# Kernel optimization log

Hardware: AMD Instinct MI355X
Metric: run time of the kernel (lower is better)

The kernel has to match this reference:

```python
import jax, jax.numpy as jnp
import numpy as np

N, E, D, G = 20000, 640000, 256, 64
BN_EPS = 1e-5


def setup_inputs() -> dict:
    key = jax.random.key(0)
    ks = jax.random.split(key, 16)
    p = lambda k, sh: jax.random.normal(k, sh, dtype=jnp.float32) * 0.05
    x = jax.random.normal(ks[0], (N, D), dtype=jnp.float32)
    edge_index = jax.random.randint(ks[1], (2, E), 0, N, dtype=jnp.int32)
    batch = jnp.sort(jax.random.randint(ks[2], (N,), 0, G, dtype=jnp.int32))
    return dict(
        x=x, edge_index=edge_index, batch=batch,
        W1=p(ks[3], (D, D)), a1_src=p(ks[4], (D,)), a1_dst=p(ks[5], (D,)), b1=p(ks[6], (D,)),
        W2=p(ks[7], (D, D)), a2_src=p(ks[8], (D,)), a2_dst=p(ks[9], (D,)), b2=p(ks[10], (D,)),
        bn_gamma=jnp.ones((D,), jnp.float32), bn_beta=jnp.zeros((D,), jnp.float32),
        bn_mean=jnp.zeros((D,), jnp.float32), bn_var=jnp.ones((D,), jnp.float32),
        Wl=p(ks[11], (D, D)), bl=p(ks[12], (D,)),
    )


def gat_conv(x, src, dst, W, a_src, a_dst, b):
    # PyG GATConv, heads=1, concat=True, negative_slope=0.2, self-loops already appended
    h = x @ W                               # [N, D]
    alpha_s = h @ a_src                     # [N]
    alpha_d = h @ a_dst                     # [N]
    e = jax.nn.leaky_relu(alpha_s[src] + alpha_d[dst], 0.2)   # [E+N]
    # segment softmax over edges grouped by destination node
    m = jax.ops.segment_max(e, dst, num_segments=N)
    ex = jnp.exp(e - m[dst])
    s = jax.ops.segment_sum(ex, dst, num_segments=N)
    alpha = ex / s[dst]                     # self-loops guarantee s > 0
    out = jax.ops.segment_sum(alpha[:, None] * h[src], dst, num_segments=N)
    return out + b


def reference(x, edge_index, batch, W1, a1_src, a1_dst, b1, W2, a2_src, a2_dst, b2,
              bn_gamma, bn_beta, bn_mean, bn_var, Wl, bl):
    loop = jnp.arange(N, dtype=edge_index.dtype)
    src = jnp.concatenate([edge_index[0], loop])
    dst = jnp.concatenate([edge_index[1], loop])

    h = jax.nn.leaky_relu(gat_conv(x, src, dst, W1, a1_src, a1_dst, b1), 0.01)
    h = jax.nn.leaky_relu(gat_conv(h, src, dst, W2, a2_src, a2_dst, b2), 0.01)
    # BatchNorm over nodes (eval mode, running stats)
    h = (h - bn_mean) * jax.lax.rsqrt(bn_var + BN_EPS) * bn_gamma + bn_beta
    # global mean pool per graph, then linear (dropout is identity in eval)
    sums = jax.ops.segment_sum(h, batch, num_segments=G)           # [G, D]
    cnt = jax.ops.segment_sum(jnp.ones((N,), h.dtype), batch, num_segments=G)
    pooled = sums / jnp.maximum(cnt, 1.0)[:, None]
    return pooled @ Wl.T + bl
```

## Files before the change

### kernel.cpp

```cpp
#include <hip/hip_runtime.h>
#include <hip/hip_bf16.h>

#define NN 20000
#define EE 640000
#define DD 256
#define GG 64
#define ETOT (EE + NN)
#define BN_EPS 1e-5f

#define NPART 8
#define PBLK  128
#define CE    (EE / PBLK)
#define PRNG  (NN / NPART)

#define GBM 64
#define GBN 128
#define GBK 64
#define NGEMMB 626
#define SCHUNKS 78
#define SCSZ 8206

typedef short s16x8 __attribute__((ext_vector_type(8)));
typedef float f32x4 __attribute__((ext_vector_type(4)));
typedef int   i32x2 __attribute__((ext_vector_type(2)));
typedef int   i32x4 __attribute__((ext_vector_type(4)));

__device__ __forceinline__ unsigned short f2bf_hi(float x) {
    unsigned u = __float_as_uint(x);
    unsigned r = (u + 0x7FFFu + ((u >> 16) & 1u)) >> 16;
    return (unsigned short)r;
}
__device__ __forceinline__ float bf2f(unsigned short h) {
    return __uint_as_float(((unsigned)h) << 16);
}

__device__ __forceinline__ void fma8o(const char* __restrict__ hbF, int boff,
                                      float a, float* acc) {
    i32x4 hv = *(const i32x4*)(hbF + boff);
    #pragma unroll
    for (int k = 0; k < 4; ++k) {
        unsigned u = (unsigned)hv[k];
        acc[2 * k]     += a * __uint_as_float(u << 16);
        acc[2 * k + 1] += a * __uint_as_float(u & 0xFFFF0000u);
    }
}

__global__ __launch_bounds__(256) void prep_hist_conv_kernel(
        const int* __restrict__ batch, int* __restrict__ start, float* __restrict__ cntf,
        const int* __restrict__ ei, int* __restrict__ counts,
        const float* __restrict__ W1, const float* __restrict__ W2,
        short* __restrict__ BhT1, short* __restrict__ BlT1,
        short* __restrict__ BhT2, short* __restrict__ BlT2) {
    int b = blockIdx.x;
    int r = b & 15, G = b >> 4;
    if (r < 8) {
        int lo = (b & 7) * PRNG;
        int e0 = G * CE;
        for (int i = e0 + threadIdx.x; i < e0 + CE; i += 256) {
            int d = ei[EE + i];
            if ((unsigned)(d - lo) < (unsigned)PRNG) atomicAdd(&counts[d], 1);
        }
        return;
    }
    int idx = G * 8 + (r - 8);
    if (idx < 512) {
        int n = idx & 255, which = idx >> 8;
        int k = threadIdx.x;
        const float* B = which ? W2 : W1;
        short* Bh = which ? BhT2 : BhT1;
        short* Bl = which ? BlT2 : BlT1;
        float x = B[k * DD + n];
        unsigned short hbv = f2bf_hi(x);
        Bh[n * DD + k] = (short)hbv;
        Bl[n * DD + k] = (short)f2bf_hi(x - bf2f(hbv));
    } else if (idx == 512) {
        int g = threadIdx.x;
        if (g <= GG) {
            if (g == GG) start[GG] = NN;
            else {
                int lo = 0, hi = NN;
                while (lo < hi) { int mid = (lo + hi) >> 1; if (batch[mid] < g) lo = mid + 1; else hi = mid; }
                start[g] = lo;
            }
        }
        __syncthreads();
        if (g < GG) cntf[g] = (float)(start[g + 1] - start[g]);
    }
}

#define SCHUNK 20
__global__ __launch_bounds__(1024) void scan_kernel(const int* __restrict__ counts,
                                                    int* __restrict__ offsets,
                                                    int* __restrict__ cursor) {
    __shared__ int wsums[16];
    int t = threadIdx.x, lane = t & 63, wid = t >> 6;
    int base = t * SCHUNK;
    int loc[SCHUNK];
    int sum = 0;
    #pragma unroll
    for (int i = 0; i < SCHUNK; ++i) {
        int idx = base + i;
        int v = (idx < NN) ? (counts[idx] + 1) : 0;
        loc[i] = sum; sum += v;
    }
    int x = sum;
    #pragma unroll
    for (int o = 1; o < 64; o <<= 1) { int tv = __shfl_up(x, o, 64); if (lane >= o) x += tv; }
    if (lane == 63) wsums[wid] = x;
    __syncthreads();
    if (wid == 0) {
        int wv = (lane < 16) ? wsums[lane] : 0;
        #pragma unroll
        for (int o = 1; o < 16; o <<= 1) { int tv = __shfl_up(wv, o, 64); if (lane >= o) wv += tv; }
        if (lane < 16) wsums[lane] = wv;
    }
    __syncthreads();
    int tbase = (wid ? wsums[wid - 1] : 0) + x - sum;
    #pragma unroll
    for (int i = 0; i < SCHUNK; ++i) {
        int idx = base + i;
        if (idx < NN) { int e = tbase + loc[i]; offsets[idx] = e; cursor[idx] = e; }
    }
    if (t == 0) offsets[NN] = wsums[15];
}

template<bool SCAT>
__global__ __launch_bounds__(256) void gemm_kernel(
        const float* __restrict__ A,
        const short* __restrict__ BhT, const short* __restrict__ BlT,
        const float* __restrict__ a_src, const float* __restrict__ a_dst,
        short* __restrict__ hb, float* __restrict__ asp, float* __restrict__ adp, int M,
        const int* __restrict__ ei, int* __restrict__ cursor, int* __restrict__ csr_src) {
    __shared__ short As_h[GBM * GBK];
    __shared__ short As_l[GBM * GBK];
    __shared__ short Bs_h[GBN * GBK];
    __shared__ short Bs_l[GBN * GBK];
    int tid = threadIdx.x;
    int lid = blockIdx.x;
    int gx = lid & 1, gy = lid >> 1;
    int row0 = gy * GBM;
    int col0 = gx * GBN;
    int w = tid >> 6, lane = tid & 63;
    int wr = w >> 1, wc = w & 1;

    f32x4 acc[2][4];
    #pragma unroll
    for (int m = 0; m < 2; ++m)
        #pragma unroll
        for (int n = 0; n < 4; ++n)
            acc[m][n] = (f32x4){0.f, 0.f, 0.f, 0.f};

    int srow = tid >> 3;
    int sslot = tid & 7;

    for (int k0 = 0; k0 < DD; k0 += GBK) {
        __syncthreads();
        #pragma unroll
        for (int p = 0; p < 2; ++p) {
            int r = p * 32 + srow;
            int gr = row0 + r;
            float xv[8];
            if (gr < M) {
                const float4* ap = (const float4*)(A + (size_t)gr * DD + k0 + sslot * 8);
                float4 a0 = ap[0], a1 = ap[1];
                xv[0] = a0.x; xv[1] = a0.y; xv[2] = a0.z; xv[3] = a0.w;
                xv[4] = a1.x; xv[5] = a1.y; xv[6] = a1.z; xv[7] = a1.w;
            } else {
                #pragma unroll
                for (int i = 0; i < 8; ++i) xv[i] = 0.f;
            }
            s16x8 hv, lv;
            #pragma unroll
            for (int i = 0; i < 8; ++i) {
                unsigned short hbb = f2bf_hi(xv[i]);
                hv[i] = (short)hbb;
                lv[i] = (short)f2bf_hi(xv[i] - bf2f(hbb));
            }
            int byte = r * 128 + ((sslot ^ (r & 7)) << 4);
            *(s16x8*)((char*)As_h + byte) = hv;
            *(s16x8*)((char*)As_l + byte) = lv;
        }
        #pragma unroll
        for (int p = 0; p < 4; ++p) {
            int r = p * 32 + srow;
            int byte = r * 128 + ((sslot ^ (r & 7)) << 4);
            const short* bhp = BhT + (size_t)(col0 + r) * DD + k0 + sslot * 8;
            const short* blp = BlT + (size_t)(col0 + r) * DD + k0 + sslot * 8;
            *(s16x8*)((char*)Bs_h + byte) = *(const s16x8*)bhp;
            *(s16x8*)((char*)Bs_l + byte) = *(const s16x8*)blp;
        }
        __syncthreads();

        #pragma unroll
        for (int ks = 0; ks < 2; ++ks) {
            s16x8 ah[2], al[2], bh[4], bl[4];
            int g = ks * 4 + (lane >> 4);
            #pragma unroll
            for (int m = 0; m < 2; ++m) {
                int r = wr * 32 + m * 16 + (lane & 15);
                int byte = r * 128 + ((g ^ (r & 7)) << 4);
                ah[m] = *(const s16x8*)((char*)As_h + byte);
                al[m] = *(const s16x8*)((char*)As_l + byte);
            }
            #pragma unroll
            for (int n = 0; n < 4; ++n) {
                int c = wc * 64 + n * 16 + (lane & 15);
                int byte = c * 128 + ((g ^ (c & 7)) << 4);
                bh[n] = *(const s16x8*)((char*)Bs_h + byte);
                bl[n] = *(const s16x8*)((char*)Bs_l + byte);
            }
            #pragma unroll
            for (int m = 0; m < 2; ++m)
                #pragma unroll
                for (int n = 0; n < 4; ++n) {
                    acc[m][n] = __builtin_amdgcn_mfma_f32_16x16x32_bf16(ah[m], bh[n], acc[m][n], 0, 0, 0);
                    acc[m][n] = __builtin_amdgcn_mfma_f32_16x16x32_bf16(ah[m], bl[n], acc[m][n], 0, 0, 0);
                    acc[m][n] = __builtin_amdgcn_mfma_f32_16x16x32_bf16(al[m], bh[n], acc[m][n], 0, 0, 0);
                }
        }
    }

    float vsrc[4], vdst[4];
    #pragma unroll
    for (int n = 0; n < 4; ++n) {
        int cg = col0 + wc * 64 + n * 16 + (lane & 15);
        vsrc[n] = a_src[cg];
        vdst[n] = a_dst[cg];
    }
    #pragma unroll
    for (int m = 0; m < 2; ++m) {
        #pragma unroll
        for (int j = 0; j < 4; ++j) {
            float ps = 0.f, pd = 0.f;
            #pragma unroll
            for (int n = 0; n < 4; ++n) {
                float c = acc[m][n][j];
                ps += c * vsrc[n];
                pd += c * vdst[n];
            }
            #pragma unroll
            for (int o = 1; o < 16; o <<= 1) {
                ps += __shfl_xor(ps, o, 64);
                pd += __shfl_xor(pd, o, 64);
            }
            if ((lane & 15) == 0) {
                int rg = row0 + wr * 32 + m * 16 + ((lane >> 4) << 2) + j;
                if (rg < M) {
                    asp[(size_t)(gx * 2 + wc) * NN + rg] = ps;
                    adp[(size_t)(gx * 2 + wc) * NN + rg] = pd;
                }
            }
        }
    }

    #pragma unroll
    for (int m = 0; m < 2; ++m) {
        int rbase = row0 + wr * 32 + m * 16 + ((lane >> 4) << 2);
        #pragma unroll
        for (int n = 0; n < 4; ++n) {
            int cg = col0 + wc * 64 + n * 16 + (lane & 15);
            #pragma unroll
            for (int j = 0; j < 4; ++j) {
                int rg = rbase + j;
                if (rg < M) hb[(size_t)rg * DD + cg] = (short)f2bf_hi(acc[m][n][j]);
            }
        }
    }

    if (SCAT && lid < SCHUNKS * NPART) {
        int part = lid & 7;
        int lo = part * PRNG;
        int e0 = (lid >> 3) * SCSZ;
        int e1 = min(e0 + SCSZ, EE);
        for (int i = e0 + tid; i < e1; i += 256) {
            int d = ei[EE + i];
            if ((unsigned)(d - lo) < (unsigned)PRNG) {
                int pos = atomicAdd(&cursor[d], 1);
                csr_src[pos] = ei[i];
            }
        }
    }
}

__global__ void reduce_kernel(const float* __restrict__ asp, const float* __restrict__ adp,
                              const int* __restrict__ offsets,
                              float* __restrict__ as_, float* __restrict__ ad_,
                              int* __restrict__ csr_src) {
    int i = blockIdx.x * blockDim.x + threadIdx.x;
    if (i < NN) {
        as_[i] = asp[i] + asp[NN + i] + asp[2 * NN + i] + asp[3 * NN + i];
        ad_[i] = adp[i] + adp[NN + i] + adp[2 * NN + i] + adp[3 * NN + i];
        csr_src[offsets[i + 1] - 1] = i;
    }
}

__global__ __launch_bounds__(256) void alpha_kernel(const int* __restrict__ csr_src,
                                                    const int* __restrict__ offsets,
                                                    const float* __restrict__ as_,
                                                    const float* __restrict__ ad_,
                                                    int2* __restrict__ pairs) {
    int tid = threadIdx.x;
    int w = tid >> 6, lane = tid & 63;
    int node = blockIdx.x * 4 + w;
    int off = offsets[node];
    int deg = offsets[node + 1] - off;
    float adn = ad_[node];

    if (deg <= 64) {
        int si = 0; float e = -INFINITY;
        if (lane < deg) {
            si = csr_src[off + lane];
            float t = as_[si] + adn;
            e = (t > 0.f) ? t : 0.2f * t;
        }
        float m = e;
        #pragma unroll
        for (int o = 32; o > 0; o >>= 1) m = fmaxf(m, __shfl_xor(m, o, 64));
        float ex = (lane < deg) ? expf(e - m) : 0.f;
        float s = ex;
        #pragma unroll
        for (int o = 32; o > 0; o >>= 1) s += __shfl_xor(s, o, 64);
        if (lane < deg) {
            int2 p; p.x = si << 9; p.y = __float_as_int(ex / s);
            pairs[off + lane] = p;
        }
        return;
    }

    float m = -INFINITY, s = 0.f;
    for (int cs = 0; cs < deg; cs += 64) {
        int cl = min(64, deg - cs);
        float e = -INFINITY;
        if (lane < cl) {
            int si = csr_src[off + cs + lane];
            float t = as_[si] + adn;
            e = (t > 0.f) ? t : 0.2f * t;
        }
        float cm = e;
        #pragma unroll
        for (int o = 32; o > 0; o >>= 1) cm = fmaxf(cm, __shfl_xor(cm, o, 64));
        float newm = fmaxf(m, cm);
        float ex = (lane < cl) ? expf(e - newm) : 0.f;
        float csum = ex;
        #pragma unroll
        for (int o = 32; o > 0; o >>= 1) csum += __shfl_xor(csum, o, 64);
        s = s * expf(m - newm) + csum;
        m = newm;
    }
    float inv = 1.f / s;
    for (int cs = 0; cs < deg; cs += 64) {
        int cl = min(64, deg - cs);
        if (lane < cl) {
            int si = csr_src[off + cs + lane];
            float t = as_[si] + adn;
            float e = (t > 0.f) ? t : 0.2f * t;
            int2 p; p.x = si << 9; p.y = __float_as_int(expf(e - m) * inv);
            pairs[off + cs + lane] = p;
        }
    }
}

__global__ __launch_bounds__(256) void aggregate_kernel(const short* __restrict__ hb,
                                                        const int2* __restrict__ pairs,
                                                        const int* __restrict__ offsets,
                                                        const float* __restrict__ bias,
                                                        float* __restrict__ out) {
    int tid = threadIdx.x;
    int w = tid >> 6, lane = tid & 63;
    int b = blockIdx.x;
    int sl = b & 3;
    int node = ((b >> 2) << 2) + w;
    int eg = lane >> 3;
    int fl = lane & 7;
    int f0 = sl * 64 + fl * 8;
    const char* hbF = (const char*)hb + f0 * 2;
    int off = offsets[node];
    int deg = offsets[node + 1] - off;
    const i32x2* pp = (const i32x2*)pairs + off;

    float accA[8], accB[8];
    #pragma unroll
    for (int k = 0; k < 8; ++k) { accA[k] = 0.f; accB[k] = 0.f; }

    int j = 0;
    i32x2 qA, qB;
    if (deg >= 16) { qA = pp[eg]; qB = pp[8 + eg]; }
    for (; j + 32 <= deg; j += 16) {
        i32x2 nA = pp[j + 16 + eg];
        i32x2 nB = pp[j + 24 + eg];
        fma8o(hbF, qA.x, __int_as_float(qA.y), accA);
        fma8o(hbF, qB.x, __int_as_float(qB.y), accB);
        qA = nA; qB = nB;
    }
    if (j + 16 <= deg) {
        fma8o(hbF, qA.x, __int_as_float(qA.y), accA);
        fma8o(hbF, qB.x, __int_as_float(qB.y), accB);
        j += 16;
    }
    {
        if (j + eg < deg) {
            i32x2 p = pp[j + eg];
            fma8o(hbF, p.x, __int_as_float(p.y), accA);
        }
        if (j + 8 + eg < deg) {
            i32x2 p = pp[j + 8 + eg];
            fma8o(hbF, p.x, __int_as_float(p.y), accB);
        }
    }

    f32x4 r0, r1;
    #pragma unroll
    for (int k = 0; k < 8; ++k) {
        float v = accA[k] + accB[k];
        v += __shfl_xor(v, 8, 64);
        v += __shfl_xor(v, 16, 64);
        v += __shfl_xor(v, 32, 64);
        if (k < 4) r0[k] = v; else r1[k - 4] = v;
    }
    if (eg == 0) {
        const f32x4 b0 = *(const f32x4*)(bias + f0);
        const f32x4 b1 = *(const f32x4*)(bias + f0 + 4);
        #pragma unroll
        for (int k = 0; k < 4; ++k) {
            float v0 = r0[k] + b0[k];
            float v1 = r1[k] + b1[k];
            r0[k] = (v0 > 0.f) ? v0 : 0.01f * v0;
            r1[k] = (v1 > 0.f) ? v1 : 0.01f * v1;
        }
        __builtin_nontemporal_store(r0, (f32x4*)(out + (size_t)node * DD + f0));
        __builtin_nontemporal_store(r1, (f32x4*)(out + (size_t)node * DD + f0 + 4));
    }
}

#define PSLICE 8
__global__ __launch_bounds__(256) void pool_kernel(const float* __restrict__ h,
                                                   const int* __restrict__ start,
                                                   float* __restrict__ pool) {
    int g = blockIdx.x >> 3, sl = blockIdx.x & (PSLICE - 1);
    int f = threadIdx.x;
    int s0 = start[g], s1 = start[g + 1];
    float acc = 0.f;
    for (int nd = s0 + sl; nd < s1; nd += PSLICE)
        acc += h[(size_t)nd * DD + f];
    if (acc != 0.f || sl == 0) atomicAdd(&pool[g * DD + f], acc);
}

__global__ __launch_bounds__(256) void final_kernel(const float* __restrict__ pool,
                                                    const float* __restrict__ cnt,
                                                    const float* __restrict__ gam,
                                                    const float* __restrict__ bet,
                                                    const float* __restrict__ mean,
                                                    const float* __restrict__ var,
                                                    const float* __restrict__ Wl,
                                                    const float* __restrict__ bl,
                                                    float* __restrict__ out) {
    __shared__ float p_sh[DD];
    int g = blockIdx.x, j = threadIdx.x;
    float cn = cnt[g];
    float scale = gam[j] * rsqrtf(var[j] + BN_EPS);
    p_sh[j] = (cn > 0.f) ? (pool[g * DD + j] / cn - mean[j]) * scale + bet[j] : 0.f;
    __syncthreads();
    float acc = 0.f;
    for (int fi = 0; fi < DD; ++fi)
        acc += p_sh[fi] * Wl[j * DD + fi];
    out[g * DD + j] = acc + bl[j];
}

extern "C" void kernel_launch(void* const* d_in, const int* in_sizes, int n_in,
                              void* d_out, int out_size, void* d_ws, size_t ws_size,
                              hipStream_t stream) {
    const float* x       = (const float*)d_in[0];
    const int*   ei      = (const int*)d_in[1];
    const int*   batch   = (const int*)d_in[2];
    const float* W1      = (const float*)d_in[3];
    const float* a1_src  = (const float*)d_in[4];
    const float* a1_dst  = (const float*)d_in[5];
    const float* b1      = (const float*)d_in[6];
    const float* W2      = (const float*)d_in[7];
    const float* a2_src  = (const float*)d_in[8];
    const float* a2_dst  = (const float*)d_in[9];
    const float* b2      = (const float*)d_in[10];
    const float* bn_g    = (const float*)d_in[11];
    const float* bn_b    = (const float*)d_in[12];
    const float* bn_m    = (const float*)d_in[13];
    const float* bn_v    = (const float*)d_in[14];
    const float* Wl      = (const float*)d_in[15];
    const float* bl      = (const float*)d_in[16];
    float* out = (float*)d_out;

    char* ws = (char*)d_ws;
    size_t o = 0;
    auto take = [&](size_t bytes) { char* p = ws + o; o += (bytes + 255) & ~(size_t)255; return p; };
    int*   counts  = (int*)  take(NN * 4);
    int*   offsets = (int*)  take((NN + 1) * 4);
    int*   cursor  = (int*)  take(NN * 4);
    int*   csr_src = (int*)  take((size_t)ETOT * 4);
    int2*  pairs   = (int2*) take((size_t)ETOT * 8);
    float* asp     = (float*)take((size_t)4 * NN * 4);
    float* adp     = (float*)take((size_t)4 * NN * 4);
    float* as_     = (float*)take(NN * 4);
    float* ad_     = (float*)take(NN * 4);
    short* hb      = (short*)take((size_t)NN * DD * 2);
    float* bufB    = (float*)take((size_t)NN * DD * 4);
    float* pool    = (float*)take(GG * DD * 4);
    float* cnt     = (float*)take(GG * 4);
    int*   start   = (int*)  take((GG + 1) * 4);
    short* BhT1    = (short*)take((size_t)DD * DD * 2);
    short* BlT1    = (short*)take((size_t)DD * DD * 2);
    short* BhT2    = (short*)take((size_t)DD * DD * 2);
    short* BlT2    = (short*)take((size_t)DD * DD * 2);
    (void)ws_size; (void)in_sizes; (void)n_in; (void)out_size;

    hipMemsetAsync(counts, 0, NN * 4, stream);
    hipMemsetAsync(pool, 0, GG * DD * 4, stream);

    prep_hist_conv_kernel<<<2048, 256, 0, stream>>>(batch, start, cnt, ei, counts,
                                                    W1, W2, BhT1, BlT1, BhT2, BlT2);
    scan_kernel<<<1, 1024, 0, stream>>>(counts, offsets, cursor);

    gemm_kernel<true><<<NGEMMB, 256, 0, stream>>>(x, BhT1, BlT1, a1_src, a1_dst,
                                                  hb, asp, adp, NN, ei, cursor, csr_src);
    reduce_kernel<<<(NN + 255) / 256, 256, 0, stream>>>(asp, adp, offsets, as_, ad_, csr_src);
    alpha_kernel<<<NN / 4, 256, 0, stream>>>(csr_src, offsets, as_, ad_, pairs);
    aggregate_kernel<<<NN, 256, 0, stream>>>(hb, pairs, offsets, b1, bufB);

    gemm_kernel<false><<<NGEMMB, 256, 0, stream>>>(bufB, BhT2, BlT2, a2_src, a2_dst,
                                                   hb, asp, adp, NN, nullptr, nullptr, nullptr);
    reduce_kernel<<<(NN + 255) / 256, 256, 0, stream>>>(asp, adp, offsets, as_, ad_, csr_src);
    alpha_kernel<<<NN / 4, 256, 0, stream>>>(csr_src, offsets, as_, ad_, pairs);
    aggregate_kernel<<<NN, 256, 0, stream>>>(hb, pairs, offsets, b2, bufB);

    pool_kernel<<<GG * PSLICE, 256, 0, stream>>>(bufB, start, pool);
    final_kernel<<<GG, 256, 0, stream>>>(pool, cnt, bn_g, bn_b, bn_m, bn_v, Wl, bl, out);
}
```

Measured before the change: 261.8 us.

## Split aggregate into 8 feature slices and use nontemporal loads/stores

The aggregation kernel now splits each node's 256 features into 8 slices of 32 instead of 4 slices of 64, and launches twice as many blocks. Each wave processes 16 edges per step instead of 8, which needs one extra shuffle stage in the reduction. Separately, many streaming global accesses (edge index reads, GEMM outputs hb/asp/adp, pairs writes and reads) become nontemporal to reduce cache pollution. The trade-off is that each edge's pair is read by twice as many blocks, and the gathered hb rows that are reused may lose cache residency.

Result: slower. 363.6 us (+38.9%).

```diff
diff --git a/kernel.cpp b/kernel.cpp
--- a/kernel.cpp
+++ b/kernel.cpp
@@ -57,7 +57,7 @@
         int lo = (b & 7) * PRNG;
         int e0 = G * CE;
         for (int i = e0 + threadIdx.x; i < e0 + CE; i += 256) {
-            int d = ei[EE + i];
+            int d = __builtin_nontemporal_load(ei + EE + i);
             if ((unsigned)(d - lo) < (unsigned)PRNG) atomicAdd(&counts[d], 1);
         }
         return;
@@ -246,8 +246,8 @@
             if ((lane & 15) == 0) {
                 int rg = row0 + wr * 32 + m * 16 + ((lane >> 4) << 2) + j;
                 if (rg < M) {
-                    asp[(size_t)(gx * 2 + wc) * NN + rg] = ps;
-                    adp[(size_t)(gx * 2 + wc) * NN + rg] = pd;
+                    __builtin_nontemporal_store(ps, &asp[(size_t)(gx * 2 + wc) * NN + rg]);
+                    __builtin_nontemporal_store(pd, &adp[(size_t)(gx * 2 + wc) * NN + rg]);
                 }
             }
         }
@@ -262,7 +262,9 @@
             #pragma unroll
             for (int j = 0; j < 4; ++j) {
                 int rg = rbase + j;
-                if (rg < M) hb[(size_t)rg * DD + cg] = (short)f2bf_hi(acc[m][n][j]);
+                if (rg < M)
+                    __builtin_nontemporal_store((short)f2bf_hi(acc[m][n][j]),
+                                                &hb[(size_t)rg * DD + cg]);
             }
         }
     }
@@ -273,10 +275,11 @@
         int e0 = (lid >> 3) * SCSZ;
         int e1 = min(e0 + SCSZ, EE);
         for (int i = e0 + tid; i < e1; i += 256) {
-            int d = ei[EE + i];
+            int d = __builtin_nontemporal_load(ei + EE + i);
             if ((unsigned)(d - lo) < (unsigned)PRNG) {
+                int s = __builtin_nontemporal_load(ei + i);
                 int pos = atomicAdd(&cursor[d], 1);
-                csr_src[pos] = ei[i];
+                csr_src[pos] = s;
             }
         }
     }
@@ -298,7 +301,7 @@
                                                     const int* __restrict__ offsets,
                                                     const float* __restrict__ as_,
                                                     const float* __restrict__ ad_,
-                                                    int2* __restrict__ pairs) {
+                                                    i32x2* __restrict__ pairs) {
     int tid = threadIdx.x;
     int w = tid >> 6, lane = tid & 63;
     int node = blockIdx.x * 4 + w;
@@ -321,8 +324,8 @@
         #pragma unroll
         for (int o = 32; o > 0; o >>= 1) s += __shfl_xor(s, o, 64);
         if (lane < deg) {
-            int2 p; p.x = si << 9; p.y = __float_as_int(ex / s);
-            pairs[off + lane] = p;
+            i32x2 p; p[0] = si << 9; p[1] = __float_as_int(ex / s);
+            __builtin_nontemporal_store(p, pairs + off + lane);
         }
         return;
     }
@@ -354,29 +357,29 @@
             int si = csr_src[off + cs + lane];
             float t = as_[si] + adn;
             float e = (t > 0.f) ? t : 0.2f * t;
-            int2 p; p.x = si << 9; p.y = __float_as_int(expf(e - m) * inv);
-            pairs[off + cs + lane] = p;
+            i32x2 p; p[0] = si << 9; p[1] = __float_as_int(expf(e - m) * inv);
+            __builtin_nontemporal_store(p, pairs + off + cs + lane);
         }
     }
 }
 
 __global__ __launch_bounds__(256) void aggregate_kernel(const short* __restrict__ hb,
-                                                        const int2* __restrict__ pairs,
+                                                        const i32x2* __restrict__ pairs,
                                                         const int* __restrict__ offsets,
                                                         const float* __restrict__ bias,
                                                         float* __restrict__ out) {
     int tid = threadIdx.x;
     int w = tid >> 6, lane = tid & 63;
     int b = blockIdx.x;
-    int sl = b & 3;
-    int node = ((b >> 2) << 2) + w;
-    int eg = lane >> 3;
-    int fl = lane & 7;
-    int f0 = sl * 64 + fl * 8;
+    int sl = b & 7;
+    int node = (b >> 3) * 4 + w;
+    int eg = lane >> 2;
+    int fl = lane & 3;
+    int f0 = sl * 32 + fl * 8;
     const char* hbF = (const char*)hb + f0 * 2;
     int off = offsets[node];
     int deg = offsets[node + 1] - off;
-    const i32x2* pp = (const i32x2*)pairs + off;
+    const i32x2* pp = pairs + off;
 
     float accA[8], accB[8];
     #pragma unroll
@@ -384,27 +387,30 @@
 
     int j = 0;
     i32x2 qA, qB;
-    if (deg >= 16) { qA = pp[eg]; qB = pp[8 + eg]; }
-    for (; j + 32 <= deg; j += 16) {
-        i32x2 nA = pp[j + 16 + eg];
-        i32x2 nB = pp[j + 24 + eg];
-        fma8o(hbF, qA.x, __int_as_float(qA.y), accA);
-        fma8o(hbF, qB.x, __int_as_float(qB.y), accB);
+    if (deg >= 32) {
+        qA = __builtin_nontemporal_load(pp + eg);
+        qB = __builtin_nontemporal_load(pp + 16 + eg);
+    }
+    for (; j + 64 <= deg; j += 32) {
+        i32x2 nA = __builtin_nontemporal_load(pp + j + 32 + eg);
+        i32x2 nB = __builtin_nontemporal_load(pp + j + 48 + eg);
+        fma8o(hbF, qA[0], __int_as_float(qA[1]), accA);
+        fma8o(hbF, qB[0], __int_as_float(qB[1]), accB);
         qA = nA; qB = nB;
     }
-    if (j + 16 <= deg) {
-        fma8o(hbF, qA.x, __int_as_float(qA.y), accA);
-        fma8o(hbF, qB.x, __int_as_float(qB.y), accB);
-        j += 16;
+    if (j + 32 <= deg) {
+        fma8o(hbF, qA[0], __int_as_float(qA[1]), accA);
+        fma8o(hbF, qB[0], __int_as_float(qB[1]), accB);
+        j += 32;
     }
     {
         if (j + eg < deg) {
-            i32x2 p = pp[j + eg];
-            fma8o(hbF, p.x, __int_as_float(p.y), accA);
-        }
-        if (j + 8 + eg < deg) {
-            i32x2 p = pp[j + 8 + eg];
-            fma8o(hbF, p.x, __int_as_float(p.y), accB);
+            i32x2 p = __builtin_nontemporal_load(pp + j + eg);
+            fma8o(hbF, p[0], __int_as_float(p[1]), accA);
+        }
+        if (j + 16 + eg < deg) {
+            i32x2 p = __builtin_nontemporal_load(pp + j + 16 + eg);
+            fma8o(hbF, p[0], __int_as_float(p[1]), accB);
         }
     }
 
@@ -412,6 +418,7 @@
     #pragma unroll
     for (int k = 0; k < 8; ++k) {
         float v = accA[k] + accB[k];
+        v += __shfl_xor(v, 4, 64);
         v += __shfl_xor(v, 8, 64);
         v += __shfl_xor(v, 16, 64);
         v += __shfl_xor(v, 32, 64);
@@ -495,7 +502,7 @@
     int*   offsets = (int*)  take((NN + 1) * 4);
     int*   cursor  = (int*)  take(NN * 4);
     int*   csr_src = (int*)  take((size_t)ETOT * 4);
-    int2*  pairs   = (int2*) take((size_t)ETOT * 8);
+    i32x2* pairs   = (i32x2*)take((size_t)ETOT * 8);
     float* asp     = (float*)take((size_t)4 * NN * 4);
     float* adp     = (float*)take((size_t)4 * NN * 4);
     float* as_     = (float*)take(NN * 4);
@@ -522,13 +529,13 @@
                                                   hb, asp, adp, NN, ei, cursor, csr_src);
     reduce_kernel<<<(NN + 255) / 256, 256, 0, stream>>>(asp, adp, offsets, as_, ad_, csr_src);
     alpha_kernel<<<NN / 4, 256, 0, stream>>>(csr_src, offsets, as_, ad_, pairs);
-    aggregate_kernel<<<NN, 256, 0, stream>>>(hb, pairs, offsets, b1, bufB);
+    aggregate_kernel<<<NN * 2, 256, 0, stream>>>(hb, pairs, offsets, b1, bufB);
 
     gemm_kernel<false><<<NGEMMB, 256, 0, stream>>>(bufB, BhT2, BlT2, a2_src, a2_dst,
                                                    hb, asp, adp, NN, nullptr, nullptr, nullptr);
     reduce_kernel<<<(NN + 255) / 256, 256, 0, stream>>>(asp, adp, offsets, as_, ad_, csr_src);
     alpha_kernel<<<NN / 4, 256, 0, stream>>>(csr_src, offsets, as_, ad_, pairs);
-    aggregate_kernel<<<NN, 256, 0, stream>>>(hb, pairs, offsets, b2, bufB);
+    aggregate_kernel<<<NN * 2, 256, 0, stream>>>(hb, pairs, offsets, b2, bufB);
 
     pool_kernel<<<GG * PSLICE, 256, 0, stream>>>(bufB, start, pool);
     final_kernel<<<GG, 256, 0, stream>>>(pool, cnt, bn_g, bn_b, bn_m, bn_v, Wl, bl, out);
```
